# Kernel tuning notes

Hardware: AMD Instinct MI355X
Metric: run time of the kernel (lower is better)

The kernel has to match this reference:

```python
import jax, jax.numpy as jnp
import numpy as np

B, T, N, C_IN = 2, 12, 50000, 1
H = 16          # hidden = out channels of STConv
KT = 3          # temporal kernel size
E = 800000      # edges (avg degree 16)
NUM_CLASSES = 2


def _temporal_conv(x, wP, bP, wQ, bQ, wR, bR):
    # Gated temporal conv (GLU): relu(P * sigmoid(Q) + R), 'valid' conv over time.
    # x: (B, Tt, N, C); w*: (KT, C, H)
    Tt = x.shape[1]
    def conv(w, b):
        out = b
        for k in range(KT):  # KT=3, tiny unrolled loop
            out = out + jnp.einsum('btnc,co->btno', x[:, k:Tt - KT + 1 + k], w[k])
        return out
    return jax.nn.relu(conv(wP, bP) * jax.nn.sigmoid(conv(wQ, bQ)) + conv(wR, bR))


def _cheb_conv(x, edge_index, edge_weight, w, b):
    # ChebConv K=2, sym normalization, lambda_max=2:
    #   out  = Tx_0 @ W0 + Tx_1 @ W1 + b
    src, dst = edge_index[0], edge_index[1]
    n = x.shape[2]
    deg = jax.ops.segment_sum(edge_weight, src, num_segments=n)
    dis = jnp.where(deg > 0, jax.lax.rsqrt(jnp.maximum(deg, 1e-12)), 0.0)
    norm = -dis[src] * edge_weight * dis[dst]                    # (E,)
    Bc, Tc, _, Hc = x.shape
    xf = jnp.transpose(x, (2, 0, 1, 3)).reshape(n, -1)           # (N, B*T*H)
    agg = jax.ops.segment_sum(norm[:, None] * xf[src], dst, num_segments=n)
    tx1 = jnp.transpose(agg.reshape(n, Bc, Tc, Hc), (1, 2, 0, 3))  # (B, T, N, H)
    return jnp.einsum('btnc,co->btno', x, w[0]) + jnp.einsum('btnc,co->btno', tx1, w[1]) + b


def _forward(x, edge_index, edge_weight,
             tc1_P_w, tc1_P_b, tc1_Q_w, tc1_Q_b, tc1_R_w, tc1_R_b,
             cheb_w, cheb_b,
             tc2_P_w, tc2_P_b, tc2_Q_w, tc2_Q_b, tc2_R_w, tc2_R_b,
             lin_w, lin_b):
    h = _temporal_conv(x, tc1_P_w, tc1_P_b, tc1_Q_w, tc1_Q_b, tc1_R_w, tc1_R_b)  # (B, T-2, N, H)
    h = jax.nn.relu(_cheb_conv(h, edge_index, edge_weight, cheb_w, cheb_b))
    h = _temporal_conv(h, tc2_P_w, tc2_P_b, tc2_Q_w, tc2_Q_b, tc2_R_w, tc2_R_b)  # (B, T-4, N, H)
    h = h.mean(axis=1)                                                            # (B, N, H)
    return h @ lin_w + lin_b                                                      # (B, N, classes)


def setup_inputs() -> dict:
    key = jax.random.key(0)
    ks = jax.random.split(key, 12)
    x = jax.random.normal(ks[0], (B, T, N, C_IN), jnp.float32)
    edge_index = jax.random.randint(ks[1], (2, E), 0, N, dtype=jnp.int32).astype(jnp.int64)
    edge_weight = jax.random.uniform(ks[2], (E,), jnp.float32)

    def conv_w(k, cin, cout):
        s = 1.0 / np.sqrt(cin * KT)
        return jax.random.uniform(k, (KT, cin, cout), jnp.float32, -s, s)

    inp = {'x': x, 'edge_index': edge_index, 'edge_weight': edge_weight}
    for i, name in enumerate(['tc1_P', 'tc1_Q', 'tc1_R']):
        inp[name + '_w'] = conv_w(ks[3 + i], C_IN, H)
        inp[name + '_b'] = jnp.zeros((H,), jnp.float32)
    for i, name in enumerate(['tc2_P', 'tc2_Q', 'tc2_R']):
        inp[name + '_w'] = conv_w(ks[6 + i], H, H)
        inp[name + '_b'] = jnp.zeros((H,), jnp.float32)
    sc = 1.0 / np.sqrt(H)
    inp['cheb_w'] = jax.random.uniform(ks[9], (2, H, H), jnp.float32, -sc, sc)
    inp['cheb_b'] = jnp.zeros((H,), jnp.float32)
    inp['lin_w'] = jax.random.uniform(ks[10], (H, NUM_CLASSES), jnp.float32, -sc, sc)
    inp['lin_b'] = jnp.zeros((NUM_CLASSES,), jnp.float32)
    return inp


def reference(x, edge_index, edge_weight,
              tc1_P_w, tc1_P_b, tc1_Q_w, tc1_Q_b, tc1_R_w, tc1_R_b,
              tc2_P_w, tc2_P_b, tc2_Q_w, tc2_Q_b, tc2_R_w, tc2_R_b,
              cheb_w, cheb_b, lin_w, lin_b):
    return _forward(x, edge_index, edge_weight,
                    tc1_P_w, tc1_P_b, tc1_Q_w, tc1_Q_b, tc1_R_w, tc1_R_b,
                    cheb_w, cheb_b,
                    tc2_P_w, tc2_P_b, tc2_Q_w, tc2_Q_b, tc2_R_w, tc2_R_b,
                    lin_w, lin_b)
```

## Files before the change

kernel.cpp:

```cpp
#include <hip/hip_runtime.h>

typedef unsigned short ushort_t;
typedef unsigned int uint_t;

constexpr int Bb = 2, Tt = 12, Nn = 50000, Hh = 16, Ee = 800000;
constexpr int T1 = 10, T2 = 8;
constexpr int F = 320;
constexpr int NP = 50176;
constexpr int CAP = 64;

#define DEV __device__ __forceinline__

DEV float bf2f(ushort_t u) { return __uint_as_float(((uint_t)u) << 16); }
DEV ushort_t f2bf(float f) {
  uint_t u = __float_as_uint(f);
  u += 0x7fffu + ((u >> 16) & 1u);
  return (ushort_t)(u >> 16);
}
DEV float blo(uint_t u) { return __uint_as_float(u << 16); }
DEV float bhi(uint_t u) { return __uint_as_float(u & 0xffff0000u); }
DEV float sigm(float x) { return 1.0f / (1.0f + __expf(-x)); }

DEV float loadF(const void* p, int j, int isb) {
  return isb ? bf2f(((const ushort_t*)p)[j]) : ((const float*)p)[j];
}
DEV int loadI(const void* p, long long j, int is64) {
  return is64 ? (int)(((const long long*)p)[j]) : ((const int*)p)[j];
}

__global__ void k_wprep(const void* ew, const void* ei,
                        const void* t1Pw, const void* t1Pb,
                        const void* t1Qw, const void* t1Qb,
                        const void* t1Rw, const void* t1Rb,
                        const void* t2Pw, const void* t2Pb,
                        const void* t2Qw, const void* t2Qb,
                        const void* t2Rw, const void* t2Rb,
                        const void* chw, const void* chb,
                        const void* lw, const void* lb,
                        int* flags, float* W) {
  __shared__ int sflags[2];
  int tid = threadIdx.x;
  if (tid < 64) {
    int lane = tid;
    const ushort_t* u = (const ushort_t*)ew;
    int cnt = 0;
    for (int j = lane; j < 512; j += 64) cnt += (u[j] < 0x3F80u) ? 1 : 0;
#pragma unroll
    for (int d = 32; d; d >>= 1) cnt += __shfl_xor(cnt, d, 64);
    const int* e32 = (const int*)ei;
    int even_nz = 0, odd_nz = 0;
    for (int j = 2 * lane; j < 256; j += 128) {
      even_nz |= (e32[j] != 0);
      odd_nz |= (e32[j + 1] != 0);
    }
    unsigned long long be = __ballot(even_nz), bo = __ballot(odd_nz);
    if (lane == 0) {
      int f0 = (cnt >= 450) ? 1 : 0;
      int f1 = (bo == 0ull && be != 0ull) ? 1 : 0;
      sflags[0] = f0; sflags[1] = f1;
      flags[0] = f0; flags[1] = f1;
    }
  }
  __syncthreads();
  int isb = sflags[0];
#define CVT(src, off, n) for (int j = tid; j < (n); j += 256) W[(off) + j] = loadF(src, j, isb);
  CVT(t1Pw, 0, 48)   CVT(t1Pb, 48, 16)
  CVT(t1Qw, 64, 48)  CVT(t1Qb, 112, 16)
  CVT(t1Rw, 128, 48) CVT(t1Rb, 176, 16)
  CVT(t2Pw, 192, 768)  CVT(t2Pb, 960, 16)
  CVT(t2Qw, 976, 768)  CVT(t2Qb, 1744, 16)
  CVT(t2Rw, 1760, 768) CVT(t2Rb, 2528, 16)
  CVT(chw, 2544, 512)  CVT(chb, 3056, 16)
  CVT(lw, 3072, 32)    CVT(lb, 3104, 2)
#undef CVT
}

__global__ __launch_bounds__(256) void k_pre(const void* __restrict__ x,
                                             const void* __restrict__ ei,
                                             const void* __restrict__ ew,
                                             const float* __restrict__ W,
                                             const int* __restrict__ flags,
                                             ushort_t* __restrict__ xfh,
                                             float* __restrict__ deg8) {
  int id = blockIdx.x * 256 + threadIdx.x;
  int isb = flags[0];
  if (id < Ee) {
    int is64 = flags[1];
    int s = loadI(ei, id, is64);
    atomicAdd(&deg8[(blockIdx.x & 7) * NP + s], loadF(ew, id, isb));
  }
  if (id < Bb * T1 * Nn) {
    int n = id % Nn;
    int bt = id / Nn;
    int t = bt % T1, b = bt / T1;
    float x0 = loadF(x, (b * Tt + t + 0) * Nn + n, isb);
    float x1 = loadF(x, (b * Tt + t + 1) * Nn + n, isb);
    float x2 = loadF(x, (b * Tt + t + 2) * Nn + n, isb);
    ushort_t g[16];
#pragma unroll
    for (int h = 0; h < 16; ++h) {
      float p = W[48 + h] + x0 * W[0 + h] + x1 * W[16 + h] + x2 * W[32 + h];
      float q = W[112 + h] + x0 * W[64 + h] + x1 * W[80 + h] + x2 * W[96 + h];
      float r = W[176 + h] + x0 * W[128 + h] + x1 * W[144 + h] + x2 * W[160 + h];
      g[h] = f2bf(fmaxf(fmaf(p, sigm(q), r), 0.0f));
    }
    uint_t u[8];
#pragma unroll
    for (int j = 0; j < 8; ++j) u[j] = (uint_t)g[2 * j] | ((uint_t)g[2 * j + 1] << 16);
    uint4* dst = (uint4*)(xfh + (size_t)n * F + t * 32 + b * 16);
    dst[0] = make_uint4(u[0], u[1], u[2], u[3]);
    dst[1] = make_uint4(u[4], u[5], u[6], u[7]);
  }
}

__global__ __launch_bounds__(256) void k_dis(float* __restrict__ deg8) {
  int i = blockIdx.x * 256 + threadIdx.x;
  if (i >= Nn) return;
  float v = 0.0f;
#pragma unroll
  for (int j = 0; j < 8; ++j) v += deg8[j * NP + i];
  deg8[i] = (v > 0.0f) ? (1.0f / sqrtf(fmaxf(v, 1e-12f))) : 0.0f;
}

__global__ __launch_bounds__(256) void k_scatter(const void* __restrict__ ei,
                                                 const void* __restrict__ ew,
                                                 const int* __restrict__ flags,
                                                 const float* __restrict__ dis,
                                                 int* __restrict__ cnt,
                                                 int2* __restrict__ ecv) {
  int e = blockIdx.x * 256 + threadIdx.x;
  if (e >= Ee) return;
  int isb = flags[0], is64 = flags[1];
  int s = loadI(ei, e, is64), d = loadI(ei, (long long)Ee + e, is64);
  float v = -dis[s] * loadF(ew, e, isb) * dis[d];
  int pos = atomicAdd(&cnt[d], 1);
  if (pos < CAP) ecv[d * CAP + pos] = make_int2(s, __float_as_int(v));
}

__global__ __launch_bounds__(256) void k_agg(const int* __restrict__ cnt,
                                             const int2* __restrict__ ecv,
                                             const uint2* __restrict__ xf2,
                                             const float* __restrict__ W,
                                             ushort_t* __restrict__ h2) {
  __shared__ float sh[4][640];
  int wid = threadIdx.x >> 6;
  int lane = threadIdx.x & 63;
  int gw = blockIdx.x * 4 + wid;
  int deg = min(cnt[gw], CAP);
  int l16 = 64 + (lane & 15);
  float a0 = 0.f, a1 = 0.f, a2 = 0.f, a3 = 0.f;
  float c0 = 0.f, c1 = 0.f, c2 = 0.f, c3 = 0.f;

#define ACC(v, p, q)                                                          \
  a0 = fmaf(v, blo(p.x), a0); a1 = fmaf(v, bhi(p.x), a1);                     \
  a2 = fmaf(v, blo(p.y), a2); a3 = fmaf(v, bhi(p.y), a3);                     \
  c0 = fmaf(v, blo(q.x), c0); c1 = fmaf(v, bhi(q.x), c1);                     \
  c2 = fmaf(v, blo(q.y), c2); c3 = fmaf(v, bhi(q.y), c3);

  int colv = 0; float valv = 0.0f;
  if (lane < deg) {
    int2 t = ecv[gw * CAP + lane];
    colv = t.x * 80;
    valv = __int_as_float(t.y);
  }
  int e = 0;
  for (; e + 4 <= deg; e += 4) {
    int r0 = __shfl(colv, e + 0), r1 = __shfl(colv, e + 1);
    int r2 = __shfl(colv, e + 2), r3 = __shfl(colv, e + 3);
    float v0 = __shfl(valv, e + 0), v1 = __shfl(valv, e + 1);
    float v2 = __shfl(valv, e + 2), v3 = __shfl(valv, e + 3);
    uint2 p0 = xf2[r0 + lane], q0 = xf2[r0 + l16];
    uint2 p1 = xf2[r1 + lane], q1 = xf2[r1 + l16];
    uint2 p2 = xf2[r2 + lane], q2 = xf2[r2 + l16];
    uint2 p3 = xf2[r3 + lane], q3 = xf2[r3 + l16];
    ACC(v0, p0, q0) ACC(v1, p1, q1) ACC(v2, p2, q2) ACC(v3, p3, q3)
  }
  for (; e < deg; ++e) {
    int r = __shfl(colv, e);
    float v = __shfl(valv, e);
    uint2 p = xf2[r + lane], q = xf2[r + l16];
    ACC(v, p, q)
  }
#undef ACC

  float* sa = sh[wid];
  float* sx = sh[wid] + 320;
  const uint2* xrow = xf2 + (size_t)gw * 80;
  uint2 xp = xrow[lane], xq = xrow[l16];
  ((float4*)sa)[lane] = make_float4(a0, a1, a2, a3);
  ((float4*)sx)[lane] = make_float4(blo(xp.x), bhi(xp.x), blo(xp.y), bhi(xp.y));
  if (lane < 16) {
    ((float4*)sa)[64 + lane] = make_float4(c0, c1, c2, c3);
    ((float4*)sx)[64 + lane] = make_float4(blo(xq.x), bhi(xq.x), blo(xq.y), bhi(xq.y));
  }
  __builtin_amdgcn_wave_barrier();
  int h = lane & 15;
  float w0[16], w1[16];
#pragma unroll
  for (int c = 0; c < 16; ++c) {
    w0[c] = W[2544 + c * 16 + h];
    w1[c] = W[2800 + c * 16 + h];
  }
  float bias = W[3056 + h];
  ushort_t* orow = h2 + (size_t)gw * F;
#pragma unroll
  for (int j = 0; j < 5; ++j) {
    int base2 = (lane & 48) + 64 * j;
    float o = bias;
#pragma unroll
    for (int c = 0; c < 16; ++c)
      o = fmaf(sx[base2 + c], w0[c], fmaf(sa[base2 + c], w1[c], o));
    orow[lane + 64 * j] = f2bf(fmaxf(o, 0.0f));
  }
}

__global__ __launch_bounds__(256) void k_tc2h(const ushort_t* __restrict__ h2,
                                              const float* __restrict__ W,
                                              float* __restrict__ out) {
  __shared__ float shh[16 * 330];
  __shared__ float sg[16 * 257];
  int tid = threadIdx.x;
  int nb = blockIdx.x * 16;

  for (int i = tid; i < 16 * 40; i += 256) {
    int node = i / 40, j = i % 40;
    uint4 q = ((const uint4*)(h2 + (size_t)(nb + node) * F))[j];
    int t = j >> 2;
    float* dstp = shh + node * 330 + t * 33 + (j & 3) * 8;
    dstp[0] = blo(q.x); dstp[1] = bhi(q.x);
    dstp[2] = blo(q.y); dstp[3] = bhi(q.y);
    dstp[4] = blo(q.z); dstp[5] = bhi(q.z);
    dstp[6] = blo(q.w); dstp[7] = bhi(q.w);
  }
  __syncthreads();

  {
    int node = tid >> 4, pair = tid & 15;
    int b = pair >> 3, t2 = pair & 7;
    const float* base = shh + node * 330 + b * 16;
    float hv[48];
#pragma unroll
    for (int k = 0; k < 3; ++k) {
      const float4* p = (const float4*)(base + (t2 + k) * 33);
      float4 e0 = p[0], e1 = p[1], e2 = p[2], e3 = p[3];
      hv[k * 16 + 0] = e0.x;  hv[k * 16 + 1] = e0.y;
      hv[k * 16 + 2] = e0.z;  hv[k * 16 + 3] = e0.w;
      hv[k * 16 + 4] = e1.x;  hv[k * 16 + 5] = e1.y;
      hv[k * 16 + 6] = e1.z;  hv[k * 16 + 7] = e1.w;
      hv[k * 16 + 8] = e2.x;  hv[k * 16 + 9] = e2.y;
      hv[k * 16 + 10] = e2.z; hv[k * 16 + 11] = e2.w;
      hv[k * 16 + 12] = e3.x; hv[k * 16 + 13] = e3.y;
      hv[k * 16 + 14] = e3.z; hv[k * 16 + 15] = e3.w;
    }
    float P[16], Q[16], R[16];
#pragma unroll
    for (int h = 0; h < 16; ++h) {
      P[h] = W[960 + h];
      Q[h] = W[1744 + h];
      R[h] = W[2528 + h];
    }
#pragma unroll
    for (int k = 0; k < 3; ++k) {
#pragma unroll
      for (int c = 0; c < 16; ++c) {
        float v = hv[k * 16 + c];
        const int wbase = k * 256 + c * 16;
#pragma unroll
        for (int h = 0; h < 16; ++h) {
          P[h] = fmaf(v, W[192 + wbase + h], P[h]);
          Q[h] = fmaf(v, W[976 + wbase + h], Q[h]);
          R[h] = fmaf(v, W[1760 + wbase + h], R[h]);
        }
      }
    }
    float* go = sg + node * 257 + pair * 16;
#pragma unroll
    for (int h = 0; h < 16; ++h)
      go[h] = fmaxf(fmaf(P[h], sigm(Q[h]), R[h]), 0.0f);
  }
  __syncthreads();

  if (tid < 32) {
    int node = tid >> 1, b = tid & 1;
    const float* gp = sg + node * 257 + b * 128;
    float mean[16];
#pragma unroll
    for (int h = 0; h < 16; ++h) mean[h] = 0.0f;
#pragma unroll
    for (int t2 = 0; t2 < T2; ++t2)
#pragma unroll
      for (int h = 0; h < 16; ++h) mean[h] += gp[t2 * 16 + h];
    float o0 = W[3104], o1 = W[3105];
#pragma unroll
    for (int h = 0; h < 16; ++h) {
      float m = mean[h] * 0.125f;
      o0 = fmaf(m, W[3072 + 2 * h], o0);
      o1 = fmaf(m, W[3072 + 2 * h + 1], o1);
    }
    ((float2*)out)[(size_t)b * Nn + nb + node] = make_float2(o0, o1);
  }
}

extern "C" void kernel_launch(void* const* d_in, const int* in_sizes, int n_in,
                              void* d_out, int out_size, void* d_ws, size_t ws_size,
                              hipStream_t stream) {
  (void)in_sizes; (void)n_in; (void)out_size; (void)ws_size;
  const void* x = d_in[0];
  const void* ei = d_in[1];
  const void* ew = d_in[2];

  char* wsb = (char*)d_ws;
  size_t off = 0;
  auto alloc = [&](size_t bytes) -> void* {
    void* p = wsb + off;
    off = (off + bytes + 255) & ~(size_t)255;
    return p;
  };
  int* flags = (int*)alloc(256);
  float* W = (float*)alloc(4096 * 4);
  float* deg8 = (float*)alloc((size_t)8 * NP * 4);
  int* cnt = (int*)alloc((size_t)NP * 4);
  int2* ecv = (int2*)alloc((size_t)Nn * CAP * 8);
  ushort_t* xfh = (ushort_t*)alloc((size_t)Nn * F * 2);
  ushort_t* h2 = (ushort_t*)alloc((size_t)Nn * F * 2);

  hipMemsetAsync(deg8, 0, (size_t)9 * NP * 4, stream);

  k_wprep<<<1, 256, 0, stream>>>(
      ew, ei,
      d_in[3], d_in[4], d_in[5], d_in[6], d_in[7], d_in[8],
      d_in[9], d_in[10], d_in[11], d_in[12], d_in[13], d_in[14],
      d_in[15], d_in[16], d_in[17], d_in[18], flags, W);

  k_pre<<<(Bb * T1 * Nn + 255) / 256, 256, 0, stream>>>(x, ei, ew, W, flags, xfh, deg8);
  k_dis<<<(Nn + 255) / 256, 256, 0, stream>>>(deg8);
  k_scatter<<<(Ee + 255) / 256, 256, 0, stream>>>(ei, ew, flags, deg8, cnt, ecv);
  k_agg<<<Nn / 4, 256, 0, stream>>>(cnt, ecv, (const uint2*)xfh, W, h2);
  k_tc2h<<<Nn / 16, 256, 0, stream>>>(h2, W, (float*)d_out);
}
```

Before: 340.5 us.

## Fuse edge bucketing into k_pre and defer normalization to aggregation

The CSR-style edge bucketing (atomic count plus ecv write) moves from a separate scatter kernel into k_pre, which already reads the edge list. Raw weights are stored, and the symmetric normalization is applied later: the source dis factor is applied per edge when ecv is loaded in k_agg, and the destination -dis factor is applied to the accumulated sums. This removes one kernel launch and a second pass over edge_index and edge_weight. The gather loop in k_agg is also unrolled from 4 to 8 edges to keep more loads in flight, at the cost of more registers. It relies on cnt being zeroed by the existing memset, which covers deg8 and the adjacent cnt region.

```diff
diff --git a/kernel.cpp b/kernel.cpp
--- a/kernel.cpp
+++ b/kernel.cpp
@@ -81,13 +81,18 @@
                                              const float* __restrict__ W,
                                              const int* __restrict__ flags,
                                              ushort_t* __restrict__ xfh,
-                                             float* __restrict__ deg8) {
+                                             float* __restrict__ deg8,
+                                             int* __restrict__ cnt,
+                                             int2* __restrict__ ecv) {
   int id = blockIdx.x * 256 + threadIdx.x;
   int isb = flags[0];
   if (id < Ee) {
     int is64 = flags[1];
-    int s = loadI(ei, id, is64);
-    atomicAdd(&deg8[(blockIdx.x & 7) * NP + s], loadF(ew, id, isb));
+    int s = loadI(ei, id, is64), d = loadI(ei, (long long)Ee + id, is64);
+    float w = loadF(ew, id, isb);
+    atomicAdd(&deg8[(blockIdx.x & 7) * NP + s], w);
+    int pos = atomicAdd(&cnt[d], 1);
+    if (pos < CAP) ecv[d * CAP + pos] = make_int2(s, __float_as_int(w));
   }
   if (id < Bb * T1 * Nn) {
     int n = id % Nn;
@@ -122,23 +127,9 @@
   deg8[i] = (v > 0.0f) ? (1.0f / sqrtf(fmaxf(v, 1e-12f))) : 0.0f;
 }
 
-__global__ __launch_bounds__(256) void k_scatter(const void* __restrict__ ei,
-                                                 const void* __restrict__ ew,
-                                                 const int* __restrict__ flags,
-                                                 const float* __restrict__ dis,
-                                                 int* __restrict__ cnt,
-                                                 int2* __restrict__ ecv) {
-  int e = blockIdx.x * 256 + threadIdx.x;
-  if (e >= Ee) return;
-  int isb = flags[0], is64 = flags[1];
-  int s = loadI(ei, e, is64), d = loadI(ei, (long long)Ee + e, is64);
-  float v = -dis[s] * loadF(ew, e, isb) * dis[d];
-  int pos = atomicAdd(&cnt[d], 1);
-  if (pos < CAP) ecv[d * CAP + pos] = make_int2(s, __float_as_int(v));
-}
-
 __global__ __launch_bounds__(256) void k_agg(const int* __restrict__ cnt,
                                              const int2* __restrict__ ecv,
+                                             const float* __restrict__ dis,
                                              const uint2* __restrict__ xf2,
                                              const float* __restrict__ W,
                                              ushort_t* __restrict__ h2) {
@@ -161,19 +152,24 @@
   if (lane < deg) {
     int2 t = ecv[gw * CAP + lane];
     colv = t.x * 80;
-    valv = __int_as_float(t.y);
+    valv = __int_as_float(t.y) * dis[t.x];
   }
   int e = 0;
-  for (; e + 4 <= deg; e += 4) {
-    int r0 = __shfl(colv, e + 0), r1 = __shfl(colv, e + 1);
-    int r2 = __shfl(colv, e + 2), r3 = __shfl(colv, e + 3);
-    float v0 = __shfl(valv, e + 0), v1 = __shfl(valv, e + 1);
-    float v2 = __shfl(valv, e + 2), v3 = __shfl(valv, e + 3);
-    uint2 p0 = xf2[r0 + lane], q0 = xf2[r0 + l16];
-    uint2 p1 = xf2[r1 + lane], q1 = xf2[r1 + l16];
-    uint2 p2 = xf2[r2 + lane], q2 = xf2[r2 + l16];
-    uint2 p3 = xf2[r3 + lane], q3 = xf2[r3 + l16];
-    ACC(v0, p0, q0) ACC(v1, p1, q1) ACC(v2, p2, q2) ACC(v3, p3, q3)
+  for (; e + 8 <= deg; e += 8) {
+    int r[8]; float v[8];
+#pragma unroll
+    for (int k = 0; k < 8; ++k) {
+      r[k] = __shfl(colv, e + k);
+      v[k] = __shfl(valv, e + k);
+    }
+    uint2 p[8], q[8];
+#pragma unroll
+    for (int k = 0; k < 8; ++k) {
+      p[k] = xf2[r[k] + lane];
+      q[k] = xf2[r[k] + l16];
+    }
+#pragma unroll
+    for (int k = 0; k < 8; ++k) { ACC(v[k], p[k], q[k]) }
   }
   for (; e < deg; ++e) {
     int r = __shfl(colv, e);
@@ -183,14 +179,15 @@
   }
 #undef ACC
 
+  float nd = -dis[gw];
   float* sa = sh[wid];
   float* sx = sh[wid] + 320;
   const uint2* xrow = xf2 + (size_t)gw * 80;
   uint2 xp = xrow[lane], xq = xrow[l16];
-  ((float4*)sa)[lane] = make_float4(a0, a1, a2, a3);
+  ((float4*)sa)[lane] = make_float4(a0 * nd, a1 * nd, a2 * nd, a3 * nd);
   ((float4*)sx)[lane] = make_float4(blo(xp.x), bhi(xp.x), blo(xp.y), bhi(xp.y));
   if (lane < 16) {
-    ((float4*)sa)[64 + lane] = make_float4(c0, c1, c2, c3);
+    ((float4*)sa)[64 + lane] = make_float4(c0 * nd, c1 * nd, c2 * nd, c3 * nd);
     ((float4*)sx)[64 + lane] = make_float4(blo(xq.x), bhi(xq.x), blo(xq.y), bhi(xq.y));
   }
   __builtin_amdgcn_wave_barrier();
@@ -332,9 +329,8 @@
       d_in[9], d_in[10], d_in[11], d_in[12], d_in[13], d_in[14],
       d_in[15], d_in[16], d_in[17], d_in[18], flags, W);
 
-  k_pre<<<(Bb * T1 * Nn + 255) / 256, 256, 0, stream>>>(x, ei, ew, W, flags, xfh, deg8);
+  k_pre<<<(Bb * T1 * Nn + 255) / 256, 256, 0, stream>>>(x, ei, ew, W, flags, xfh, deg8, cnt, ecv);
   k_dis<<<(Nn + 255) / 256, 256, 0, stream>>>(deg8);
-  k_scatter<<<(Ee + 255) / 256, 256, 0, stream>>>(ei, ew, flags, deg8, cnt, ecv);
-  k_agg<<<Nn / 4, 256, 0, stream>>>(cnt, ecv, (const uint2*)xfh, W, h2);
+  k_agg<<<Nn / 4, 256, 0, stream>>>(cnt, ecv, deg8, (const uint2*)xfh, W, h2);
   k_tc2h<<<Nn / 16, 256, 0, stream>>>(h2, W, (float*)d_out);
 }
```

After: 347.9 us. 1.02x slower.

## Fuse edge bucketing into preprocessing kernel with per-XCD buckets and deferred normalization

Applied to the files above, without the earlier changes.

Edge bucketing by destination now happens inside the preprocessing kernel, using eight per-XCD count and bucket arrays so atomics stay local, and the separate scatter kernel is removed. The symmetric normalization is split: the source-side factor is applied when gathering bucket entries in the aggregation kernel, and the destination-side factor scales the accumulated sum. The memset is replaced by zeroing inside the widened weight-prep launch. In exchange, each per-XCD bucket is capped at 20 entries and the merged degree is truncated at 64, which can silently drop edges for high-degree nodes.

```diff
diff --git a/kernel.cpp b/kernel.cpp
--- a/kernel.cpp
+++ b/kernel.cpp
@@ -7,7 +7,7 @@
 constexpr int T1 = 10, T2 = 8;
 constexpr int F = 320;
 constexpr int NP = 50176;
-constexpr int CAP = 64;
+constexpr int CAP = 20;
 
 #define DEV __device__ __forceinline__
 
@@ -37,7 +37,11 @@
                         const void* t2Rw, const void* t2Rb,
                         const void* chw, const void* chb,
                         const void* lw, const void* lb,
-                        int* flags, float* W) {
+                        int* flags, float* W, uint_t* zero_base) {
+  int gid = blockIdx.x * 256 + threadIdx.x;
+  if (gid < 16 * NP) zero_base[gid] = 0u;
+  if (blockIdx.x != 0) return;
+
   __shared__ int sflags[2];
   int tid = threadIdx.x;
   if (tid < 64) {
@@ -81,13 +85,19 @@
                                              const float* __restrict__ W,
                                              const int* __restrict__ flags,
                                              ushort_t* __restrict__ xfh,
-                                             float* __restrict__ deg8) {
+                                             float* __restrict__ deg8,
+                                             int* __restrict__ cnt8,
+                                             int2* __restrict__ ecv8) {
   int id = blockIdx.x * 256 + threadIdx.x;
   int isb = flags[0];
   if (id < Ee) {
     int is64 = flags[1];
-    int s = loadI(ei, id, is64);
-    atomicAdd(&deg8[(blockIdx.x & 7) * NP + s], loadF(ew, id, isb));
+    int xcd = blockIdx.x & 7;
+    int s = loadI(ei, id, is64), d = loadI(ei, (long long)Ee + id, is64);
+    float w = loadF(ew, id, isb);
+    atomicAdd(&deg8[xcd * NP + s], w);
+    int pos = atomicAdd(&cnt8[xcd * NP + d], 1);
+    if (pos < CAP) ecv8[(size_t)xcd * Nn * CAP + d * CAP + pos] = make_int2(s, __float_as_int(w));
   }
   if (id < Bb * T1 * Nn) {
     int n = id % Nn;
@@ -122,23 +132,9 @@
   deg8[i] = (v > 0.0f) ? (1.0f / sqrtf(fmaxf(v, 1e-12f))) : 0.0f;
 }
 
-__global__ __launch_bounds__(256) void k_scatter(const void* __restrict__ ei,
-                                                 const void* __restrict__ ew,
-                                                 const int* __restrict__ flags,
-                                                 const float* __restrict__ dis,
-                                                 int* __restrict__ cnt,
-                                                 int2* __restrict__ ecv) {
-  int e = blockIdx.x * 256 + threadIdx.x;
-  if (e >= Ee) return;
-  int isb = flags[0], is64 = flags[1];
-  int s = loadI(ei, e, is64), d = loadI(ei, (long long)Ee + e, is64);
-  float v = -dis[s] * loadF(ew, e, isb) * dis[d];
-  int pos = atomicAdd(&cnt[d], 1);
-  if (pos < CAP) ecv[d * CAP + pos] = make_int2(s, __float_as_int(v));
-}
-
-__global__ __launch_bounds__(256) void k_agg(const int* __restrict__ cnt,
-                                             const int2* __restrict__ ecv,
+__global__ __launch_bounds__(256) void k_agg(const int* __restrict__ cnt8,
+                                             const int2* __restrict__ ecv8,
+                                             const float* __restrict__ dis,
                                              const uint2* __restrict__ xf2,
                                              const float* __restrict__ W,
                                              ushort_t* __restrict__ h2) {
@@ -146,8 +142,22 @@
   int wid = threadIdx.x >> 6;
   int lane = threadIdx.x & 63;
   int gw = blockIdx.x * 4 + wid;
-  int deg = min(cnt[gw], CAP);
   int l16 = 64 + (lane & 15);
+
+  int colv = 0; float valv = 0.0f;
+  int o = 0;
+#pragma unroll
+  for (int j = 0; j < 8; ++j) {
+    int cj = min(cnt8[j * NP + gw], CAP);
+    if (lane >= o && lane < o + cj) {
+      int2 t = ecv8[(size_t)j * Nn * CAP + gw * CAP + (lane - o)];
+      colv = t.x * 80;
+      valv = __int_as_float(t.y) * dis[t.x];
+    }
+    o += cj;
+  }
+  int deg = min(o, 64);
+
   float a0 = 0.f, a1 = 0.f, a2 = 0.f, a3 = 0.f;
   float c0 = 0.f, c1 = 0.f, c2 = 0.f, c3 = 0.f;
 
@@ -157,12 +167,6 @@
   c0 = fmaf(v, blo(q.x), c0); c1 = fmaf(v, bhi(q.x), c1);                     \
   c2 = fmaf(v, blo(q.y), c2); c3 = fmaf(v, bhi(q.y), c3);
 
-  int colv = 0; float valv = 0.0f;
-  if (lane < deg) {
-    int2 t = ecv[gw * CAP + lane];
-    colv = t.x * 80;
-    valv = __int_as_float(t.y);
-  }
   int e = 0;
   for (; e + 4 <= deg; e += 4) {
     int r0 = __shfl(colv, e + 0), r1 = __shfl(colv, e + 1);
@@ -183,14 +187,15 @@
   }
 #undef ACC
 
+  float nd = -dis[gw];
   float* sa = sh[wid];
   float* sx = sh[wid] + 320;
   const uint2* xrow = xf2 + (size_t)gw * 80;
   uint2 xp = xrow[lane], xq = xrow[l16];
-  ((float4*)sa)[lane] = make_float4(a0, a1, a2, a3);
+  ((float4*)sa)[lane] = make_float4(a0 * nd, a1 * nd, a2 * nd, a3 * nd);
   ((float4*)sx)[lane] = make_float4(blo(xp.x), bhi(xp.x), blo(xp.y), bhi(xp.y));
   if (lane < 16) {
-    ((float4*)sa)[64 + lane] = make_float4(c0, c1, c2, c3);
+    ((float4*)sa)[64 + lane] = make_float4(c0 * nd, c1 * nd, c2 * nd, c3 * nd);
     ((float4*)sx)[64 + lane] = make_float4(blo(xq.x), bhi(xq.x), blo(xq.y), bhi(xq.y));
   }
   __builtin_amdgcn_wave_barrier();
@@ -206,11 +211,11 @@
 #pragma unroll
   for (int j = 0; j < 5; ++j) {
     int base2 = (lane & 48) + 64 * j;
-    float o = bias;
+    float o2 = bias;
 #pragma unroll
     for (int c = 0; c < 16; ++c)
-      o = fmaf(sx[base2 + c], w0[c], fmaf(sa[base2 + c], w1[c], o));
-    orow[lane + 64 * j] = f2bf(fmaxf(o, 0.0f));
+      o2 = fmaf(sx[base2 + c], w0[c], fmaf(sa[base2 + c], w1[c], o2));
+    orow[lane + 64 * j] = f2bf(fmaxf(o2, 0.0f));
   }
 }
 
@@ -319,22 +324,20 @@
   int* flags = (int*)alloc(256);
   float* W = (float*)alloc(4096 * 4);
   float* deg8 = (float*)alloc((size_t)8 * NP * 4);
-  int* cnt = (int*)alloc((size_t)NP * 4);
-  int2* ecv = (int2*)alloc((size_t)Nn * CAP * 8);
+  int* cnt8 = (int*)alloc((size_t)8 * NP * 4);
+  int2* ecv8 = (int2*)alloc((size_t)8 * Nn * CAP * 8);
   ushort_t* xfh = (ushort_t*)alloc((size_t)Nn * F * 2);
   ushort_t* h2 = (ushort_t*)alloc((size_t)Nn * F * 2);
 
-  hipMemsetAsync(deg8, 0, (size_t)9 * NP * 4, stream);
-
-  k_wprep<<<1, 256, 0, stream>>>(
+  int zblk = (16 * NP + 255) / 256;
+  k_wprep<<<zblk, 256, 0, stream>>>(
       ew, ei,
       d_in[3], d_in[4], d_in[5], d_in[6], d_in[7], d_in[8],
       d_in[9], d_in[10], d_in[11], d_in[12], d_in[13], d_in[14],
-      d_in[15], d_in[16], d_in[17], d_in[18], flags, W);
-
-  k_pre<<<(Bb * T1 * Nn + 255) / 256, 256, 0, stream>>>(x, ei, ew, W, flags, xfh, deg8);
+      d_in[15], d_in[16], d_in[17], d_in[18], flags, W, (uint_t*)deg8);
+
+  k_pre<<<(Bb * T1 * Nn + 255) / 256, 256, 0, stream>>>(x, ei, ew, W, flags, xfh, deg8, cnt8, ecv8);
   k_dis<<<(Nn + 255) / 256, 256, 0, stream>>>(deg8);
-  k_scatter<<<(Ee + 255) / 256, 256, 0, stream>>>(ei, ew, flags, deg8, cnt, ecv);
-  k_agg<<<Nn / 4, 256, 0, stream>>>(cnt, ecv, (const uint2*)xfh, W, h2);
+  k_agg<<<Nn / 4, 256, 0, stream>>>(cnt8, ecv8, deg8, (const uint2*)xfh, W, h2);
   k_tc2h<<<Nn / 16, 256, 0, stream>>>(h2, W, (float*)d_out);
 }
```

Result: slower. 370.0 us (+8.7%).
